# Kernel tuning notes

Measured on AMD Instinct MI355X. Metric: run time of the kernel, lower is better.

Reference implementation:

```python
import jax, jax.numpy as jnp
import numpy as np


def setup_inputs() -> dict:
    key = jax.random.key(0)
    kx, ky = jax.random.split(key)
    B, N, M, D = 8, 4096, 4096, 128
    x = jax.random.normal(kx, (B, N, D), dtype=jnp.float32)
    y = jax.random.normal(ky, (B, M, D), dtype=jnp.float32)
    return {"x": x, "y": y}


def reference(x, y):
    # Pairwise L2 distances, equivalent to torch.cdist(x, y) (p=2).
    # ||x_i - y_j||^2 = ||x_i||^2 + ||y_j||^2 - 2 <x_i, y_j>
    x2 = jnp.sum(x * x, axis=-1)[:, :, None]          # [B, N, 1]
    y2 = jnp.sum(y * y, axis=-1)[:, None, :]          # [B, 1, M]
    xy = jnp.einsum("bnd,bmd->bnm", x, y)             # [B, N, M]
    D = jnp.sqrt(jnp.maximum(x2 + y2 - 2.0 * xy, 0.0))  # [B, N, M]
    coverage = D.min(axis=1).mean(axis=-1)            # min over N -> [B, M] -> [B]
    precision = D.min(axis=2).mean(axis=-1)           # min over M -> [B, N] -> [B]
    return (coverage + precision).mean()              # scalar Chamfer loss
```

## Files before the change

### kernel.cpp

```cpp
#include <hip/hip_runtime.h>
#include <cstdint>


#define B_   8
#define N_   4096
#define M_   4096
#define D_   128
#define TPB  8
#define ROWS_PB 256
#define XG   (N_ / ROWS_PB)
#define CHUNKS (M_ / (TPB * 64))

typedef __bf16 bf16x8 __attribute__((ext_vector_type(8)));
typedef float  f32x4  __attribute__((ext_vector_type(4)));
typedef unsigned int u32;

static __device__ __forceinline__ unsigned short f2bf(float f) {
  unsigned u = __float_as_uint(f);
  u += 0x7FFFu + ((u >> 16) & 1u);
  return (unsigned short)(u >> 16);
}

static __device__ __forceinline__ void gld16(void* lds, const void* g) {
  __builtin_amdgcn_global_load_lds(
      (const __attribute__((address_space(1))) void*)g,
      (__attribute__((address_space(3))) void*)lds, 16, 0, 0);
}

__global__ __launch_bounds__(256) void pass1_prep(
    const float* __restrict__ x, const float* __restrict__ y,
    unsigned short* __restrict__ xb, unsigned short* __restrict__ yb,
    float* __restrict__ x2, float* __restrict__ y2,
    float* __restrict__ rowmin, float* __restrict__ colmin)
{
  const int ROWS = B_ * N_;
  int gw   = (blockIdx.x * 256 + threadIdx.x) >> 6;
  int lane = threadIdx.x & 63;
  int half = lane >> 5, sub = lane & 31;
  int row2 = gw * 2 + half;
  bool isx = row2 < ROWS;
  const float* src; unsigned short* dst; float* nrm; float* minp; int row;
  if (isx) { src = x; dst = xb; nrm = x2; minp = rowmin; row = row2; }
  else     { src = y; dst = yb; nrm = y2; minp = colmin; row = row2 - ROWS; }
  size_t base = (size_t)row * D_ + sub * 4;
  float4 v = *(const float4*)(src + base);
  float sx = isx ? -2.0f : 1.0f;
  u32 p0 = (u32)f2bf(sx * v.x) | ((u32)f2bf(sx * v.y) << 16);
  u32 p1 = (u32)f2bf(sx * v.z) | ((u32)f2bf(sx * v.w) << 16);
  *(uint2*)(dst + base) = make_uint2(p0, p1);
  float s = v.x * v.x + v.y * v.y + v.z * v.z + v.w * v.w;
  #pragma unroll
  for (int m = 1; m < 32; m <<= 1) s += __shfl_xor(s, m, 64);
  if (sub == 0)      nrm[row]  = s;
  else if (sub == 1) minp[row] = __uint_as_float(0x7F800000u);
}

__global__ __launch_bounds__(256) void pass2_tile(
    const unsigned short* __restrict__ xb, const unsigned short* __restrict__ yb,
    const float* __restrict__ x2, const float* __restrict__ y2,
    float* __restrict__ rowmin, float* __restrict__ colmin)
{
  __shared__ unsigned short ys[2 * 8192];

  const int tid  = threadIdx.x;
  const int wave = tid >> 6;
  const int lane = tid & 63;
  const int quad = lane >> 4;
  const int l15  = lane & 15;

  const int id    = blockIdx.x;
  const int b     = id & 7;
  const int xg    = (id >> 3) & 15;
  const int chunk = id >> 7;
  const int n0    = xg * ROWS_PB;
  const int mc0   = chunk * (TPB * 64);

  int srcoff[4], ldsoff[4];
  #pragma unroll
  for (int i = 0; i < 4; ++i) {
    int p  = (wave * 4 + i) * 1024 + lane * 16;
    int r  = p >> 8;
    int pc = (p >> 4) & 15;
    int c  = pc ^ (r & 15);
    srcoff[i] = r * D_ + c * 8;
    ldsoff[i] = (wave * 4 + i) * 1024;
  }

  {
    const unsigned short* src = yb + ((size_t)b * M_ + mc0) * D_;
    #pragma unroll
    for (int i = 0; i < 4; ++i) gld16((char*)ys + ldsoff[i], src + srcoff[i]);
  }

  bf16x8 afrag[4][4];
  const size_t xrow0 = (size_t)b * N_ + n0 + wave * 64;
  #pragma unroll
  for (int kb = 0; kb < 4; ++kb)
    #pragma unroll
    for (int rt = 0; rt < 4; ++rt)
      afrag[kb][rt] = *(const bf16x8*)(xb + (xrow0 + rt * 16 + l15) * D_ + kb * 32 + quad * 8);

  f32x4 xvv[4];
  #pragma unroll
  for (int rt = 0; rt < 4; ++rt)
    #pragma unroll
    for (int r = 0; r < 4; ++r)
      xvv[rt][r] = x2[(size_t)b * N_ + n0 + wave * 64 + rt * 16 + quad * 4 + r];

  const float FINF = __uint_as_float(0x7F800000u);
  float rmin2[4][4];
  #pragma unroll
  for (int rt = 0; rt < 4; ++rt)
    #pragma unroll
    for (int r = 0; r < 4; ++r) rmin2[rt][r] = FINF;

  #pragma unroll 1
  for (int t = 0; t < TPB; ++t) {
    const int m0 = mc0 + t * 64;
    const int d  = (t & 1) * 16384;
    __syncthreads();

    if (t + 1 < TPB) {
      const unsigned short* src = yb + ((size_t)b * M_ + m0 + 64) * D_;
      char* dst = (char*)ys + (16384 - d);
      #pragma unroll
      for (int i = 0; i < 4; ++i) gld16(dst + ldsoff[i], src + srcoff[i]);
    }

    float y2r[4];
    #pragma unroll
    for (int ct = 0; ct < 4; ++ct)
      y2r[ct] = y2[(size_t)b * M_ + m0 + ct * 16 + l15];

    #pragma unroll
    for (int ct = 0; ct < 4; ++ct) {
      bf16x8 bfr[4];
      #pragma unroll
      for (int kb = 0; kb < 4; ++kb) {
        const int row = ct * 16 + l15;
        const int pcB = (kb * 4 + quad) ^ l15;
        bfr[kb] = *(const bf16x8*)((const char*)ys + d + row * 256 + pcB * 16);
      }
      f32x4 a[4];
      #pragma unroll
      for (int rt = 0; rt < 4; ++rt) a[rt] = xvv[rt];
      __builtin_amdgcn_s_setprio(1);
      #pragma unroll
      for (int kb = 0; kb < 4; ++kb)
        #pragma unroll
        for (int rt = 0; rt < 4; ++rt)
          a[rt] = __builtin_amdgcn_mfma_f32_16x16x32_bf16(afrag[kb][rt], bfr[kb], a[rt], 0, 0, 0);
      __builtin_amdgcn_s_setprio(0);

      float yv = y2r[ct];
      float c[4];
      #pragma unroll
      for (int rt = 0; rt < 4; ++rt) {
        float s0 = a[rt][0] + yv; rmin2[rt][0] = fminf(rmin2[rt][0], s0);
        float s1 = a[rt][1] + yv; rmin2[rt][1] = fminf(rmin2[rt][1], s1);
        float s2 = a[rt][2] + yv; rmin2[rt][2] = fminf(rmin2[rt][2], s2);
        float s3 = a[rt][3] + yv; rmin2[rt][3] = fminf(rmin2[rt][3], s3);
        c[rt] = fminf(fminf(s0, s1), fminf(s2, s3));
      }
      float cm = fminf(fminf(c[0], c[1]), fminf(c[2], c[3]));
      cm = fminf(cm, __shfl_xor(cm, 16, 64));
      cm = fminf(cm, __shfl_xor(cm, 32, 64));
      if (quad == 0)
        atomicMin((int*)(colmin + (size_t)b * M_ + m0 + ct * 16 + l15),
                  __float_as_int(cm));
    }
  }

  #pragma unroll
  for (int rt = 0; rt < 4; ++rt) {
    #pragma unroll
    for (int r = 0; r < 4; ++r) {
      float v = rmin2[rt][r];
      v = fminf(v, __shfl_xor(v, 1, 64));
      v = fminf(v, __shfl_xor(v, 2, 64));
      v = fminf(v, __shfl_xor(v, 4, 64));
      v = fminf(v, __shfl_xor(v, 8, 64));
      if (l15 == 0)
        atomicMin((int*)(rowmin + (size_t)b * N_ + n0 + wave * 64 + rt * 16 + quad * 4 + r),
                  __float_as_int(v));
    }
  }
}

__global__ __launch_bounds__(256) void pass3_final(
    const float* __restrict__ rowmin, const float* __restrict__ colmin,
    float* __restrict__ out)
{
  const int BN = B_ * N_;
  float s1 = 0.0f, s2 = 0.0f;
  for (int i = blockIdx.x * 256 + threadIdx.x; i < BN; i += 64 * 256) {
    s1 += sqrtf(fmaxf(rowmin[i], 0.0f));
    s2 += sqrtf(fmaxf(colmin[i], 0.0f));
  }
  float s = s1 + s2;
  #pragma unroll
  for (int m = 1; m < 64; m <<= 1) s += __shfl_xor(s, m, 64);
  __shared__ float r1[4];
  int wave = threadIdx.x >> 6, lane = threadIdx.x & 63;
  if (lane == 0) r1[wave] = s;
  __syncthreads();
  if (threadIdx.x == 0)
    atomicAdd(out, (r1[0] + r1[1] + r1[2] + r1[3]) / (float)(B_ * N_));
}

extern "C" void kernel_launch(void* const* d_in, const int* in_sizes, int n_in,
                              void* d_out, int out_size, void* d_ws, size_t ws_size,
                              hipStream_t stream)
{
  const float* x = (const float*)d_in[0];
  const float* y = (const float*)d_in[1];
  char* ws = (char*)d_ws;

  unsigned short* xb = (unsigned short*)(ws);
  unsigned short* yb = (unsigned short*)(ws + (8u << 20));
  float* x2     = (float*)(ws + (16u << 20));
  float* y2     = (float*)(ws + (16u << 20) + (1u << 17));
  float* rowmin = (float*)(ws + (16u << 20) + (2u << 17));
  float* colmin = (float*)(ws + (16u << 20) + (3u << 17));
  float* outf = (float*)d_out;

  hipMemsetAsync(outf, 0, sizeof(float), stream);

  pass1_prep<<<(B_ * N_) / 4, 256, 0, stream>>>(x, y, xb, yb, x2, y2, rowmin, colmin);

  pass2_tile<<<B_ * XG * CHUNKS, 256, 0, stream>>>(xb, yb, x2, y2, rowmin, colmin);

  pass3_final<<<64, 256, 0, stream>>>(rowmin, colmin, outf);
}
```

Before: 127.6 us.

## Fuse x conversion into tile kernel and final reduction via last-block counter

The x-side bf16 conversion and squared-norm computation move into the main tile kernel, which now reads fp32 x directly and builds MFMA A fragments in registers. The separate final reduction kernel and the output memset are replaced by a last-block-done atomic counter inside the tile kernel. The B-fragment LDS loads are interleaved with the MFMAs and the setprio hints are dropped. This cuts two launches and the xb/x2 round-trip through memory, at the cost of redundant x conversion across the chunk blocks and a serial final reduction done by a single block.

```diff
diff --git a/kernel.cpp b/kernel.cpp
--- a/kernel.cpp
+++ b/kernel.cpp
@@ -10,6 +10,7 @@
 #define ROWS_PB 256
 #define XG   (N_ / ROWS_PB)
 #define CHUNKS (M_ / (TPB * 64))
+#define GRID (B_ * XG * CHUNKS)
 
 typedef __bf16 bf16x8 __attribute__((ext_vector_type(8)));
 typedef float  f32x4  __attribute__((ext_vector_type(4)));
@@ -20,47 +21,49 @@
   u += 0x7FFFu + ((u >> 16) & 1u);
   return (unsigned short)(u >> 16);
 }
-
+static __device__ __forceinline__ u32 pk2(float a, float b) {
+  return (u32)f2bf(a) | ((u32)f2bf(b) << 16);
+}
 static __device__ __forceinline__ void gld16(void* lds, const void* g) {
   __builtin_amdgcn_global_load_lds(
       (const __attribute__((address_space(1))) void*)g,
       (__attribute__((address_space(3))) void*)lds, 16, 0, 0);
 }
 
-__global__ __launch_bounds__(256) void pass1_prep(
-    const float* __restrict__ x, const float* __restrict__ y,
-    unsigned short* __restrict__ xb, unsigned short* __restrict__ yb,
-    float* __restrict__ x2, float* __restrict__ y2,
-    float* __restrict__ rowmin, float* __restrict__ colmin)
+__global__ __launch_bounds__(256) void prep_y(
+    const float* __restrict__ y, unsigned short* __restrict__ yb,
+    float* __restrict__ y2, float* __restrict__ minbuf, int* __restrict__ counter)
 {
-  const int ROWS = B_ * N_;
-  int gw   = (blockIdx.x * 256 + threadIdx.x) >> 6;
+  const int flat = blockIdx.x * 256 + threadIdx.x;
+  if (flat < 2 * B_ * N_) minbuf[flat] = __uint_as_float(0x7F800000u);
+  if (flat == 0) *counter = 0;
+
+  int gw   = flat >> 6;
   int lane = threadIdx.x & 63;
   int half = lane >> 5, sub = lane & 31;
-  int row2 = gw * 2 + half;
-  bool isx = row2 < ROWS;
-  const float* src; unsigned short* dst; float* nrm; float* minp; int row;
-  if (isx) { src = x; dst = xb; nrm = x2; minp = rowmin; row = row2; }
-  else     { src = y; dst = yb; nrm = y2; minp = colmin; row = row2 - ROWS; }
+  int row  = gw * 2 + half;
   size_t base = (size_t)row * D_ + sub * 4;
-  float4 v = *(const float4*)(src + base);
-  float sx = isx ? -2.0f : 1.0f;
-  u32 p0 = (u32)f2bf(sx * v.x) | ((u32)f2bf(sx * v.y) << 16);
-  u32 p1 = (u32)f2bf(sx * v.z) | ((u32)f2bf(sx * v.w) << 16);
-  *(uint2*)(dst + base) = make_uint2(p0, p1);
+  float4 v = *(const float4*)(y + base);
+  u32 p0 = pk2(v.x, v.y);
+  u32 p1 = pk2(v.z, v.w);
+  *(uint2*)(yb + base) = make_uint2(p0, p1);
   float s = v.x * v.x + v.y * v.y + v.z * v.z + v.w * v.w;
   #pragma unroll
   for (int m = 1; m < 32; m <<= 1) s += __shfl_xor(s, m, 64);
-  if (sub == 0)      nrm[row]  = s;
-  else if (sub == 1) minp[row] = __uint_as_float(0x7F800000u);
-}
-
-__global__ __launch_bounds__(256) void pass2_tile(
-    const unsigned short* __restrict__ xb, const unsigned short* __restrict__ yb,
-    const float* __restrict__ x2, const float* __restrict__ y2,
-    float* __restrict__ rowmin, float* __restrict__ colmin)
+  if (sub == 0) y2[row] = s;
+}
+
+__global__ __launch_bounds__(256) void chamfer(
+    const float* __restrict__ x, const unsigned short* __restrict__ yb,
+    const float* __restrict__ y2, float* __restrict__ minbuf,
+    int* __restrict__ counter, float* __restrict__ out)
 {
   __shared__ unsigned short ys[2 * 8192];
+  __shared__ int amLast;
+  __shared__ float red[4];
+
+  float* rowmin = minbuf;
+  float* colmin = minbuf + B_ * N_;
 
   const int tid  = threadIdx.x;
   const int wave = tid >> 6;
@@ -93,19 +96,36 @@
   }
 
   bf16x8 afrag[4][4];
-  const size_t xrow0 = (size_t)b * N_ + n0 + wave * 64;
-  #pragma unroll
-  for (int kb = 0; kb < 4; ++kb)
+  f32x4 xvv[4];
+  {
+    float x2row[4];
+    #pragma unroll
+    for (int rt = 0; rt < 4; ++rt) {
+      const float* xs = x + (size_t)(b * N_ + n0 + wave * 64 + rt * 16 + l15) * D_ + quad * 8;
+      float p = 0.0f;
+      #pragma unroll
+      for (int kb = 0; kb < 4; ++kb) {
+        float4 u0 = *(const float4*)(xs + kb * 32);
+        float4 u1 = *(const float4*)(xs + kb * 32 + 4);
+        p += u0.x*u0.x + u0.y*u0.y + u0.z*u0.z + u0.w*u0.w
+           + u1.x*u1.x + u1.y*u1.y + u1.z*u1.z + u1.w*u1.w;
+        union { u32 w[4]; bf16x8 v; } tt;
+        tt.w[0] = pk2(-2.f*u0.x, -2.f*u0.y);
+        tt.w[1] = pk2(-2.f*u0.z, -2.f*u0.w);
+        tt.w[2] = pk2(-2.f*u1.x, -2.f*u1.y);
+        tt.w[3] = pk2(-2.f*u1.z, -2.f*u1.w);
+        afrag[kb][rt] = tt.v;
+      }
+      p += __shfl_xor(p, 16, 64);
+      p += __shfl_xor(p, 32, 64);
+      x2row[rt] = p;
+    }
     #pragma unroll
     for (int rt = 0; rt < 4; ++rt)
-      afrag[kb][rt] = *(const bf16x8*)(xb + (xrow0 + rt * 16 + l15) * D_ + kb * 32 + quad * 8);
-
-  f32x4 xvv[4];
-  #pragma unroll
-  for (int rt = 0; rt < 4; ++rt)
-    #pragma unroll
-    for (int r = 0; r < 4; ++r)
-      xvv[rt][r] = x2[(size_t)b * N_ + n0 + wave * 64 + rt * 16 + quad * 4 + r];
+      #pragma unroll
+      for (int r = 0; r < 4; ++r)
+        xvv[rt][r] = __shfl(x2row[rt], quad * 4 + r, 16);
+  }
 
   const float FINF = __uint_as_float(0x7F800000u);
   float rmin2[4][4];
@@ -134,24 +154,18 @@
 
     #pragma unroll
     for (int ct = 0; ct < 4; ++ct) {
-      bf16x8 bfr[4];
+      f32x4 a[4];
+      #pragma unroll
+      for (int rt = 0; rt < 4; ++rt) a[rt] = xvv[rt];
       #pragma unroll
       for (int kb = 0; kb < 4; ++kb) {
         const int row = ct * 16 + l15;
         const int pcB = (kb * 4 + quad) ^ l15;
-        bfr[kb] = *(const bf16x8*)((const char*)ys + d + row * 256 + pcB * 16);
-      }
-      f32x4 a[4];
-      #pragma unroll
-      for (int rt = 0; rt < 4; ++rt) a[rt] = xvv[rt];
-      __builtin_amdgcn_s_setprio(1);
-      #pragma unroll
-      for (int kb = 0; kb < 4; ++kb)
+        bf16x8 bfr = *(const bf16x8*)((const char*)ys + d + row * 256 + pcB * 16);
         #pragma unroll
         for (int rt = 0; rt < 4; ++rt)
-          a[rt] = __builtin_amdgcn_mfma_f32_16x16x32_bf16(afrag[kb][rt], bfr[kb], a[rt], 0, 0, 0);
-      __builtin_amdgcn_s_setprio(0);
-
+          a[rt] = __builtin_amdgcn_mfma_f32_16x16x32_bf16(afrag[kb][rt], bfr, a[rt], 0, 0, 0);
+      }
       float yv = y2r[ct];
       float c[4];
       #pragma unroll
@@ -185,27 +199,26 @@
                   __float_as_int(v));
     }
   }
-}
-
-__global__ __launch_bounds__(256) void pass3_final(
-    const float* __restrict__ rowmin, const float* __restrict__ colmin,
-    float* __restrict__ out)
-{
-  const int BN = B_ * N_;
-  float s1 = 0.0f, s2 = 0.0f;
-  for (int i = blockIdx.x * 256 + threadIdx.x; i < BN; i += 64 * 256) {
-    s1 += sqrtf(fmaxf(rowmin[i], 0.0f));
-    s2 += sqrtf(fmaxf(colmin[i], 0.0f));
-  }
-  float s = s1 + s2;
-  #pragma unroll
-  for (int m = 1; m < 64; m <<= 1) s += __shfl_xor(s, m, 64);
-  __shared__ float r1[4];
-  int wave = threadIdx.x >> 6, lane = threadIdx.x & 63;
-  if (lane == 0) r1[wave] = s;
+
+  __threadfence();
   __syncthreads();
-  if (threadIdx.x == 0)
-    atomicAdd(out, (r1[0] + r1[1] + r1[2] + r1[3]) / (float)(B_ * N_));
+  if (tid == 0) amLast = (atomicAdd(counter, 1) == GRID - 1);
+  __syncthreads();
+  if (amLast) {
+    __threadfence();
+    float s = 0.0f;
+    for (int i = tid; i < 2 * B_ * N_; i += 256) {
+      float v = __hip_atomic_load(minbuf + i, __ATOMIC_RELAXED,
+                                  __HIP_MEMORY_SCOPE_AGENT);
+      s += sqrtf(fmaxf(v, 0.0f));
+    }
+    #pragma unroll
+    for (int m = 1; m < 64; m <<= 1) s += __shfl_xor(s, m, 64);
+    if (lane == 0) red[wave] = s;
+    __syncthreads();
+    if (tid == 0)
+      *out = (red[0] + red[1] + red[2] + red[3]) / (float)(B_ * N_);
+  }
 }
 
 extern "C" void kernel_launch(void* const* d_in, const int* in_sizes, int n_in,
@@ -216,19 +229,13 @@
   const float* y = (const float*)d_in[1];
   char* ws = (char*)d_ws;
 
-  unsigned short* xb = (unsigned short*)(ws);
-  unsigned short* yb = (unsigned short*)(ws + (8u << 20));
-  float* x2     = (float*)(ws + (16u << 20));
-  float* y2     = (float*)(ws + (16u << 20) + (1u << 17));
-  float* rowmin = (float*)(ws + (16u << 20) + (2u << 17));
-  float* colmin = (float*)(ws + (16u << 20) + (3u << 17));
+  unsigned short* yb = (unsigned short*)(ws);
+  float* y2     = (float*)(ws + (8u << 20));
+  float* minbuf = (float*)(ws + (8u << 20) + (1u << 17));
+  int*   cnt    = (int*)  (ws + (8u << 20) + (3u << 17));
   float* outf = (float*)d_out;
 
-  hipMemsetAsync(outf, 0, sizeof(float), stream);
-
-  pass1_prep<<<(B_ * N_) / 4, 256, 0, stream>>>(x, y, xb, yb, x2, y2, rowmin, colmin);
-
-  pass2_tile<<<B_ * XG * CHUNKS, 256, 0, stream>>>(xb, yb, x2, y2, rowmin, colmin);
-
-  pass3_final<<<64, 256, 0, stream>>>(rowmin, colmin, outf);
-}
+  prep_y<<<(B_ * M_) / 8, 256, 0, stream>>>(y, yb, y2, minbuf, cnt);
+
+  chamfer<<<GRID, 256, 0, stream>>>(x, yb, y2, minbuf, cnt, outf);
+}
```

After: 259.0 us. 103% more time.

## Fuse final reduction into tile kernel via last-block counter, drop memset

Applied to the files above, without the earlier changes.

Removes the separate final-reduction kernel and the output memset. The last block to finish, detected with an atomic counter, now sums sqrt of the row and column minima and writes the result directly. The prep kernel initialises the min buffers and resets the counter. The MFMA inner loop is also reordered so each B fragment is loaded just before its MFMAs, and the s_setprio hints are dropped, which changes register pressure and scheduling. This saves launch overhead, but the final sum is now done by a single block, which serialises that tail work.

```diff
diff --git a/kernel.cpp b/kernel.cpp
--- a/kernel.cpp
+++ b/kernel.cpp
@@ -10,6 +10,7 @@
 #define ROWS_PB 256
 #define XG   (N_ / ROWS_PB)
 #define CHUNKS (M_ / (TPB * 64))
+#define GRID (B_ * XG * CHUNKS)
 
 typedef __bf16 bf16x8 __attribute__((ext_vector_type(8)));
 typedef float  f32x4  __attribute__((ext_vector_type(4)));
@@ -20,28 +21,31 @@
   u += 0x7FFFu + ((u >> 16) & 1u);
   return (unsigned short)(u >> 16);
 }
-
 static __device__ __forceinline__ void gld16(void* lds, const void* g) {
   __builtin_amdgcn_global_load_lds(
       (const __attribute__((address_space(1))) void*)g,
       (__attribute__((address_space(3))) void*)lds, 16, 0, 0);
 }
 
-__global__ __launch_bounds__(256) void pass1_prep(
+__global__ __launch_bounds__(256) void prep(
     const float* __restrict__ x, const float* __restrict__ y,
     unsigned short* __restrict__ xb, unsigned short* __restrict__ yb,
     float* __restrict__ x2, float* __restrict__ y2,
-    float* __restrict__ rowmin, float* __restrict__ colmin)
+    float* __restrict__ minbuf, int* __restrict__ counter)
 {
   const int ROWS = B_ * N_;
-  int gw   = (blockIdx.x * 256 + threadIdx.x) >> 6;
+  const int flat = blockIdx.x * 256 + threadIdx.x;
+  if (flat < 2 * B_ * N_) minbuf[flat] = __uint_as_float(0x7F800000u);
+  if (flat == 0) *counter = 0;
+
+  int gw   = flat >> 6;
   int lane = threadIdx.x & 63;
   int half = lane >> 5, sub = lane & 31;
   int row2 = gw * 2 + half;
   bool isx = row2 < ROWS;
-  const float* src; unsigned short* dst; float* nrm; float* minp; int row;
-  if (isx) { src = x; dst = xb; nrm = x2; minp = rowmin; row = row2; }
-  else     { src = y; dst = yb; nrm = y2; minp = colmin; row = row2 - ROWS; }
+  const float* src; unsigned short* dst; float* nrm; int row;
+  if (isx) { src = x; dst = xb; nrm = x2; row = row2; }
+  else     { src = y; dst = yb; nrm = y2; row = row2 - ROWS; }
   size_t base = (size_t)row * D_ + sub * 4;
   float4 v = *(const float4*)(src + base);
   float sx = isx ? -2.0f : 1.0f;
@@ -51,16 +55,21 @@
   float s = v.x * v.x + v.y * v.y + v.z * v.z + v.w * v.w;
   #pragma unroll
   for (int m = 1; m < 32; m <<= 1) s += __shfl_xor(s, m, 64);
-  if (sub == 0)      nrm[row]  = s;
-  else if (sub == 1) minp[row] = __uint_as_float(0x7F800000u);
-}
-
-__global__ __launch_bounds__(256) void pass2_tile(
+  if (sub == 0) nrm[row] = s;
+}
+
+__global__ __launch_bounds__(256) void chamfer(
     const unsigned short* __restrict__ xb, const unsigned short* __restrict__ yb,
     const float* __restrict__ x2, const float* __restrict__ y2,
-    float* __restrict__ rowmin, float* __restrict__ colmin)
+    float* __restrict__ minbuf, int* __restrict__ counter,
+    float* __restrict__ out)
 {
   __shared__ unsigned short ys[2 * 8192];
+  __shared__ int amLast;
+  __shared__ float red[4];
+
+  float* rowmin = minbuf;
+  float* colmin = minbuf + B_ * N_;
 
   const int tid  = threadIdx.x;
   const int wave = tid >> 6;
@@ -134,24 +143,18 @@
 
     #pragma unroll
     for (int ct = 0; ct < 4; ++ct) {
-      bf16x8 bfr[4];
+      f32x4 a[4];
+      #pragma unroll
+      for (int rt = 0; rt < 4; ++rt) a[rt] = xvv[rt];
       #pragma unroll
       for (int kb = 0; kb < 4; ++kb) {
         const int row = ct * 16 + l15;
         const int pcB = (kb * 4 + quad) ^ l15;
-        bfr[kb] = *(const bf16x8*)((const char*)ys + d + row * 256 + pcB * 16);
-      }
-      f32x4 a[4];
-      #pragma unroll
-      for (int rt = 0; rt < 4; ++rt) a[rt] = xvv[rt];
-      __builtin_amdgcn_s_setprio(1);
-      #pragma unroll
-      for (int kb = 0; kb < 4; ++kb)
+        bf16x8 bfr = *(const bf16x8*)((const char*)ys + d + row * 256 + pcB * 16);
         #pragma unroll
         for (int rt = 0; rt < 4; ++rt)
-          a[rt] = __builtin_amdgcn_mfma_f32_16x16x32_bf16(afrag[kb][rt], bfr[kb], a[rt], 0, 0, 0);
-      __builtin_amdgcn_s_setprio(0);
-
+          a[rt] = __builtin_amdgcn_mfma_f32_16x16x32_bf16(afrag[kb][rt], bfr, a[rt], 0, 0, 0);
+      }
       float yv = y2r[ct];
       float c[4];
       #pragma unroll
@@ -185,27 +188,29 @@
                   __float_as_int(v));
     }
   }
-}
-
-__global__ __launch_bounds__(256) void pass3_final(
-    const float* __restrict__ rowmin, const float* __restrict__ colmin,
-    float* __restrict__ out)
-{
-  const int BN = B_ * N_;
-  float s1 = 0.0f, s2 = 0.0f;
-  for (int i = blockIdx.x * 256 + threadIdx.x; i < BN; i += 64 * 256) {
-    s1 += sqrtf(fmaxf(rowmin[i], 0.0f));
-    s2 += sqrtf(fmaxf(colmin[i], 0.0f));
-  }
-  float s = s1 + s2;
-  #pragma unroll
-  for (int m = 1; m < 64; m <<= 1) s += __shfl_xor(s, m, 64);
-  __shared__ float r1[4];
-  int wave = threadIdx.x >> 6, lane = threadIdx.x & 63;
-  if (lane == 0) r1[wave] = s;
+
   __syncthreads();
-  if (threadIdx.x == 0)
-    atomicAdd(out, (r1[0] + r1[1] + r1[2] + r1[3]) / (float)(B_ * N_));
+  if (tid == 0)
+    amLast = (__hip_atomic_fetch_add(counter, 1, __ATOMIC_RELAXED,
+                                     __HIP_MEMORY_SCOPE_AGENT) == GRID - 1);
+  __syncthreads();
+  if (amLast) {
+    __threadfence();
+    const float4* mb4 = (const float4*)minbuf;
+    float s = 0.0f;
+    #pragma unroll 4
+    for (int i = tid; i < (2 * B_ * N_) / 4; i += 256) {
+      float4 v = mb4[i];
+      s += sqrtf(fmaxf(v.x, 0.0f)) + sqrtf(fmaxf(v.y, 0.0f))
+         + sqrtf(fmaxf(v.z, 0.0f)) + sqrtf(fmaxf(v.w, 0.0f));
+    }
+    #pragma unroll
+    for (int m = 1; m < 64; m <<= 1) s += __shfl_xor(s, m, 64);
+    if (lane == 0) red[wave] = s;
+    __syncthreads();
+    if (tid == 0)
+      *out = (red[0] + red[1] + red[2] + red[3]) / (float)(B_ * N_);
+  }
 }
 
 extern "C" void kernel_launch(void* const* d_in, const int* in_sizes, int n_in,
@@ -220,15 +225,12 @@
   unsigned short* yb = (unsigned short*)(ws + (8u << 20));
   float* x2     = (float*)(ws + (16u << 20));
   float* y2     = (float*)(ws + (16u << 20) + (1u << 17));
-  float* rowmin = (float*)(ws + (16u << 20) + (2u << 17));
-  float* colmin = (float*)(ws + (16u << 20) + (3u << 17));
+  float* minbuf = (float*)(ws + (16u << 20) + (2u << 17));
+  int*   cnt    = (int*)  (ws + (16u << 20) + (4u << 17));
   float* outf = (float*)d_out;
 
-  hipMemsetAsync(outf, 0, sizeof(float), stream);
-
-  pass1_prep<<<(B_ * N_) / 4, 256, 0, stream>>>(x, y, xb, yb, x2, y2, rowmin, colmin);
-
-  pass2_tile<<<B_ * XG * CHUNKS, 256, 0, stream>>>(xb, yb, x2, y2, rowmin, colmin);
-
-  pass3_final<<<64, 256, 0, stream>>>(rowmin, colmin, outf);
-}
+
+  prep<<<(B_ * N_) / 4, 256, 0, stream>>>(x, y, xb, yb, x2, y2, minbuf, cnt);
+
+  chamfer<<<GRID, 256, 0, stream>>>(xb, yb, x2, y2, minbuf, cnt, outf);
+}
```

New measurement: 145.1 us. 1.14x slower.
